# Kernel optimization log

Hardware: AMD Instinct MI355X
Metric: run time of the kernel (lower is better)

## Reference

```python
import jax, jax.numpy as jnp
import numpy as np

B, L, D, H = 4, 1024, 1024, 16
HD = D // H
TERM = 20  # N-term / C-term window size


def setup_inputs() -> dict:
    key = jax.random.key(0)
    ks = jax.random.split(key, 9)
    x = jax.random.normal(ks[0], (B, L, D), jnp.float32)
    lens = jax.random.randint(ks[1], (B,), 64, L + 1)
    mask = jnp.arange(L)[None, :] < lens[:, None]  # contiguous valid prefix, bool [B,L]
    s = 0.02  # ~ xavier_uniform with gain 1/H**0.25
    Wq = jax.random.normal(ks[2], (D, D), jnp.float32) * s
    Wk = jax.random.normal(ks[3], (D, D), jnp.float32) * s
    Wv = jax.random.normal(ks[4], (D, D), jnp.float32) * s
    bq = jnp.zeros((D,), jnp.float32)
    bk = jnp.zeros((D,), jnp.float32)
    bv = jnp.zeros((D,), jnp.float32)
    gamma = jnp.ones((D,), jnp.float32)
    beta = jnp.zeros((D,), jnp.float32)
    return {"x": x, "mask": mask, "Wq": Wq, "bq": bq, "Wk": Wk, "bk": bk,
            "Wv": Wv, "bv": bv, "gamma": gamma, "beta": beta}


def reference(x, mask, Wq, bq, Wk, bk, Wv, bv, gamma, beta):
    # LayerNorm (eps = 1e-5, torch default)
    mu = x.mean(-1, keepdims=True)
    var = ((x - mu) ** 2).mean(-1, keepdims=True)
    xn = (x - mu) / jnp.sqrt(var + 1e-5) * gamma + beta

    Q = (xn @ Wq + bq).reshape(B, L, H, HD)
    K = (xn @ Wk + bk).reshape(B, L, H, HD)
    V = (xn @ Wv + bv).reshape(B, L, H, HD)

    # note: original divides by head_dim**0.25 (quarter power) - keep faithful
    scores = jnp.einsum('bqhd,bkhd->bhqk', Q, K) / HD ** 0.25

    # mask fill on key positions
    scores = jnp.where(mask[:, None, None, :], scores, -10000.0)

    # per-sample length-dependent bias on key positions
    lens = mask.sum(-1)                      # [B] int
    pos = jnp.arange(L)                      # [L]
    inlen = pos[None, :] < lens[:, None]     # [B,L]
    bias_ge = (1.0 * (pos[None, :] < TERM)
               + 0.8 * ((pos[None, :] >= lens[:, None] - TERM) & inlen))
    bias_lt = (1.0 + 0.8) * inlen
    bias = jnp.where((lens >= TERM)[:, None], bias_ge, bias_lt)  # [B,L]
    scores = scores + bias[:, None, None, :]

    attn = jax.nn.softmax(scores, axis=-1)   # [B,H,L,L]
    entropy_loss = -(attn * jnp.log(attn + 1e-10)).sum(-1).mean()

    context = jnp.einsum('bhqk,bkhd->bqhd', attn, V).reshape(B, L, D)

    # ragged N-term / C-term mean pooling (vectorized segment means)
    term = jnp.minimum(TERM, lens)           # [B]
    termf = term.astype(x.dtype)[:, None]
    wn = (pos[None, :] < term[:, None]).astype(x.dtype)                      # first term tokens
    wc = ((pos[None, :] >= (lens - term)[:, None]) & inlen).astype(x.dtype)  # last term valid tokens
    n_term = (context * wn[:, :, None]).sum(1) / termf
    c_term = (context * wc[:, :, None]).sum(1) / termf
    global_pool = context.mean(1)            # mean over full L, as in original

    pooled = jnp.concatenate([n_term, c_term, global_pool], axis=1)  # [B,3D]
    return pooled, attn.mean(1), entropy_loss
```

## Files before the change

kernel.cpp:

```cpp
#include <hip/hip_runtime.h>
#include <hip/hip_bf16.h>
#include <hip/hip_fp16.h>


typedef unsigned short u16;
typedef __attribute__((ext_vector_type(4))) float f32x4;
typedef __attribute__((ext_vector_type(8))) __bf16 bf16x8;
typedef __attribute__((ext_vector_type(4))) unsigned int u32x4;
typedef __attribute__((ext_vector_type(4))) unsigned short u16x4;
typedef __attribute__((ext_vector_type(8))) unsigned short u16x8;

typedef const __attribute__((address_space(1))) unsigned int* gas1;
typedef __attribute__((address_space(3))) unsigned int* las3;

#define DEV __device__ __forceinline__

DEV float bf2f(u16 u){ union{unsigned i; float f;} c; c.i = ((unsigned)u)<<16; return c.f; }
DEV u16 f2bf(float f){ union{float f; unsigned i;} c; c.f=f; unsigned i=c.i;
  unsigned r = i + 0x7FFFu + ((i>>16)&1u); return (u16)(r>>16); }

__global__ void k_detect(const void* mask, const void* gamma, const void* beta,
                         const void* bq, const void* bk, const void* bv,
                         int* lens, float* ent, int* flag,
                         u16* gam_c, u16* bet_c, u16* bq_c, u16* bk_c, u16* bv_c,
                         float* pacc){
  int t = threadIdx.x; int w = t>>6; int lane = t&63;
  int isf32 = (((const u16*)gamma)[0] == 0) ? 1 : 0;
  if (t==0){ *flag = isf32; *ent = 0.f; }
  for (int i=t; i<12288; i+=256) pacc[i] = 0.f;
  for (int i=t; i<1024; i+=256){
    if (isf32){
      gam_c[i]=f2bf(((const float*)gamma)[i]); bet_c[i]=f2bf(((const float*)beta)[i]);
      bq_c[i] =f2bf(((const float*)bq)[i]);    bk_c[i] =f2bf(((const float*)bk)[i]);
      bv_c[i] =f2bf(((const float*)bv)[i]);
    } else {
      gam_c[i]=((const u16*)gamma)[i]; bet_c[i]=((const u16*)beta)[i];
      bq_c[i] =((const u16*)bq)[i];    bk_c[i] =((const u16*)bk)[i];
      bv_c[i] =((const u16*)bv)[i];
    }
  }
  const unsigned char* mb = (const unsigned char*)mask;
  const int* mi = (const int*)mask;
  const u16* ms = (const u16*)mask;
  int cnt = 0;
  if (mb[1] != 0) {
    if (mb[0]==1 && mb[1]==1) { for (int i=lane;i<1024;i+=64) cnt += (mb[w*1024+i]!=0); }
    else                      { for (int i=lane;i<1024;i+=64) cnt += (ms[w*1024+i]!=0); }
  } else {
    if (mi[1]==0)             { for (int i=lane;i<1024;i+=64) cnt += (mi[(w*1024+i)*2]!=0); }
    else                      { for (int i=lane;i<1024;i+=64) cnt += (mi[w*1024+i]!=0); }
  }
  #pragma unroll
  for (int o=32;o;o>>=1) cnt += __shfl_down(cnt,o);
  if (lane==0) lens[w] = cnt;
}

DEV void tr64_body(const void* src, u16* dst, int R, int C, int bt, int isf32, int t,
                   u16 (*tile)[68]){
  int tc_n = C>>6;
  int tr = (bt / tc_n)<<6, tc = (bt % tc_n)<<6;
  if (isf32){
    const float* s = (const float*)src;
    #pragma unroll
    for (int it=0; it<2; ++it){
      int f = it*2048 + t*8; int r=f>>6, c=f&63;
      const float* p = s + (long)(tr+r)*C + tc + c;
      f32x4 a = *(const f32x4*)p, b = *(const f32x4*)(p+4);
      u16x4 ua, ub;
      #pragma unroll
      for (int j=0;j<4;j++){ ua[j]=f2bf(a[j]); ub[j]=f2bf(b[j]); }
      *(u16x4*)&tile[r][c]   = ua;
      *(u16x4*)&tile[r][c+4] = ub;
    }
  } else {
    const u16* s = (const u16*)src;
    #pragma unroll
    for (int it=0; it<2; ++it){
      int f = it*2048 + t*8; int r=f>>6, c=f&63;
      *(u16x4*)&tile[r][c]   = *(const u16x4*)(s + (long)(tr+r)*C + tc + c);
      *(u16x4*)&tile[r][c+4] = *(const u16x4*)(s + (long)(tr+r)*C + tc + c + 4);
    }
  }
  __syncthreads();
  #pragma unroll
  for (int it=0; it<2; ++it){
    int f = it*2048 + t*8; int r=f>>6, c=f&63;
    u16x4 a, b2;
    #pragma unroll
    for (int j=0;j<4;j++){ a[j]=tile[c+j][r]; b2[j]=tile[c+4+j][r]; }
    *(u16x4*)(dst + (long)(tc+r)*R + tr + c)     = a;
    *(u16x4*)(dst + (long)(tc+r)*R + tr + c + 4) = b2;
  }
}

__global__ __launch_bounds__(256) void k_prep(const void* x, const u16* gamma, const u16* beta,
    u16* xn, const void* Wq, const void* Wk, const void* Wv, u16* Wt, const int* flagp){
  __shared__ u16 tile[64][68];
  int isf32 = *flagp;
  int id = blockIdx.x, t = threadIdx.x;
  if (id < 4096){
    int row = id;
    float f0,f1,f2,f3;
    if (isf32){
      f32x4 v = ((const f32x4*)x)[(size_t)row*256 + t];
      f0=v[0]; f1=v[1]; f2=v[2]; f3=v[3];
    } else {
      u16x4 v = ((const u16x4*)x)[(size_t)row*256 + t];
      f0=bf2f(v[0]); f1=bf2f(v[1]); f2=bf2f(v[2]); f3=bf2f(v[3]);
    }
    float s = f0+f1+f2+f3;
    float sq = f0*f0+f1*f1+f2*f2+f3*f3;
    #pragma unroll
    for (int o=32;o;o>>=1){ s += __shfl_down(s,o); sq += __shfl_down(sq,o); }
    float* rs = (float*)&tile[0][0];
    float* rq = rs + 4;
    if ((t&63)==0){ rs[t>>6]=s; rq[t>>6]=sq; }
    __syncthreads();
    s = rs[0]+rs[1]+rs[2]+rs[3]; sq = rq[0]+rq[1]+rq[2]+rq[3];
    float mu = s*(1.0f/1024.0f);
    float var = sq*(1.0f/1024.0f) - mu*mu;
    float rstd = rsqrtf(var + 1e-5f);
    u16x4 gv = ((const u16x4*)gamma)[t];
    u16x4 bv = ((const u16x4*)beta)[t];
    u16x4 o;
    o[0]=f2bf((f0-mu)*rstd*bf2f(gv[0])+bf2f(bv[0]));
    o[1]=f2bf((f1-mu)*rstd*bf2f(gv[1])+bf2f(bv[1]));
    o[2]=f2bf((f2-mu)*rstd*bf2f(gv[2])+bf2f(bv[2]));
    o[3]=f2bf((f3-mu)*rstd*bf2f(gv[3])+bf2f(bv[3]));
    ((u16x4*)(xn + (size_t)row*1024))[t] = o;
  } else {
    int bt = id - 4096;
    int sub = bt >> 8, tl = bt & 255;
    const void* src = (sub==0) ? Wq : (sub==1) ? Wk : Wv;
    tr64_body(src, Wt + ((size_t)sub<<20), 1024, 1024, tl, isf32, t, tile);
  }
}

__global__ __launch_bounds__(256) void k_trV(const u16* Vb, u16* Vt){
  __shared__ u16 tile[64][68];
  tr64_body(Vb + ((size_t)blockIdx.y<<16), Vt + ((size_t)blockIdx.y<<16),
            1024, 64, blockIdx.x, 0, threadIdx.x, tile);
}

__global__ __launch_bounds__(256) void k_gemm(const u16* A, const u16* Bt,
    const u16* biasq, const u16* biask, const u16* biasv,
    u16* Qb, u16* Kb, u16* Vb, const int* lens){
  int m0 = (blockIdx.x & 31)<<7;
  int n0 = (int)(blockIdx.x >> 5)<<7;
  if (n0 >= 1024 && (m0 & 1023) >= lens[m0>>10]) return;
  __shared__ u16 lA[2][4096];
  __shared__ u16 lB[2][4096];
  int t = threadIdx.x;
  int w = t>>6, l = t&63, g = l>>4, lc = l&15;
  int wm = w>>1, wn = w&1;
  int fb0 = t*16, fb1 = 4096 + t*16;
  int r0 = fb0>>6, c0 = fb0&63, r1 = fb1>>6, c1 = fb1&63;
  const char* Ab = (const char*)A; const char* Bb = (const char*)Bt;
  long aoff0 = (long)(m0+r0)*2048 + c0;
  long aoff1 = (long)(m0+r1)*2048 + c1;
  long boff0 = (long)(n0+r0)*2048 + c0;
  long boff1 = (long)(n0+r1)*2048 + c1;
  int lw = w<<10;

  #define STAGEK(buf, ko) do{ \
    __builtin_amdgcn_global_load_lds((gas1)(const void*)(Ab + aoff0 + (ko)), \
        (las3)(void*)((char*)&lA[buf][0] + lw), 16, 0, 0); \
    __builtin_amdgcn_global_load_lds((gas1)(const void*)(Ab + aoff1 + (ko)), \
        (las3)(void*)((char*)&lA[buf][0] + 4096 + lw), 16, 0, 0); \
    __builtin_amdgcn_global_load_lds((gas1)(const void*)(Bb + boff0 + (ko)), \
        (las3)(void*)((char*)&lB[buf][0] + lw), 16, 0, 0); \
    __builtin_amdgcn_global_load_lds((gas1)(const void*)(Bb + boff1 + (ko)), \
        (las3)(void*)((char*)&lB[buf][0] + 4096 + lw), 16, 0, 0); \
  }while(0)

  f32x4 vzero = {0.f,0.f,0.f,0.f};
  f32x4 acc[4][4];
  #pragma unroll
  for (int i=0;i<4;i++)
    #pragma unroll
    for (int j=0;j<4;j++) acc[i][j] = vzero;

  STAGEK(0, 0);
  __syncthreads();
  for (int kt=0; kt<32; ++kt){
    int cur = kt & 1;
    if (kt < 31) STAGEK(cur^1, (long)(kt+1)*64);
    bf16x8 af[4], bfr[4];
    #pragma unroll
    for (int i=0;i<4;i++) af[i]  = *(const bf16x8*)(const void*)&lA[cur][((wm<<6)+(i<<4)+lc)*32 + (g<<3)];
    #pragma unroll
    for (int j=0;j<4;j++) bfr[j] = *(const bf16x8*)(const void*)&lB[cur][((wn<<6)+(j<<4)+lc)*32 + (g<<3)];
    #pragma unroll
    for (int i=0;i<4;i++)
      #pragma unroll
      for (int j=0;j<4;j++)
        acc[i][j] = __builtin_amdgcn_mfma_f32_16x16x32_bf16(af[i], bfr[j], acc[i][j], 0,0,0);
    __syncthreads();
  }
  #undef STAGEK
  #pragma unroll
  for (int j=0;j<4;j++){
    int n = n0 + (wn<<6) + (j<<4) + lc;
    int kind = n>>10; int nn = n & 1023;
    const u16* bp = (kind==0)?biasq:(kind==1)?biask:biasv;
    float bvl = bf2f(bp[nn]);
    u16* dst = (kind==0)?Qb:(kind==1)?Kb:Vb;
    int h = nn>>6, hd = n&63;
    #pragma unroll
    for (int i=0;i<4;i++){
      #pragma unroll
      for (int r=0;r<4;r++){
        int m = m0 + (wm<<6) + (i<<4) + (g<<2) + r;
        int bb = m>>10, pos = m&1023;
        dst[(((bb<<4)+h)<<16) + (pos<<6) + hd] = f2bf(acc[i][j][r] + bvl);
      }
    }
  }
}

__global__ __launch_bounds__(512) void k_attn(const u16* Qg, const u16* Kg, const u16* Vt,
    const int* lens, u16* ctx, u16* Pp, float* ent_acc){
  __shared__ u16 Plds[16][1032];
  __shared__ float redz[16][8];
  __shared__ float rede[16][8];
  __shared__ __half redc[2][16][66];
  int bqi = blockIdx.x;
  int qt = bqi & 63, hg = (bqi>>6)&3, b = bqi>>8;
  int q0 = qt<<4;
  int t = threadIdx.x, w = t>>6, l = t&63, g = l>>4, lc = l&15;
  int kh = w>>2, dg = w&3;
  int len = lens[b];
  {
    u16x8 z8 = {0,0,0,0,0,0,0,0};
    u16* pz = &Plds[0][0];
    for (int i=t; i<2064; i+=512) *(u16x8*)(pz + i*8) = z8;
  }
  __half2 mh[8][2];
  #pragma unroll
  for (int i=0;i<8;i++){ mh[i][0] = __float2half2_rn(0.f); mh[i][1] = __float2half2_rn(0.f); }
  float ent_local = 0.f;
  const float SCALE = 0.35355339059327373f;
  for (int hh=0; hh<4; ++hh){
    int h = (hg<<2) + hh;
    int base = ((b<<4)+h)<<16;
    bf16x8 qf0 = *(const bf16x8*)(const void*)(Qg + base + ((q0+lc)<<6) + (g<<3));
    bf16x8 qf1 = *(const bf16x8*)(const void*)(Qg + base + ((q0+lc)<<6) + (g<<3) + 32);
    f32x4 s[8];
    float zp[4]={0,0,0,0}, ep[4]={0,0,0,0};
    #pragma unroll
    for (int tt=0; tt<8; ++tt){
      int kb = (tt<<7)+(w<<4);
      if (kb < len){
        const u16* kp = Kg + base + ((kb+lc)<<6) + (g<<3);
        bf16x8 kf0 = *(const bf16x8*)(const void*)kp;
        bf16x8 kf1 = *(const bf16x8*)(const void*)(kp + 32);
        f32x4 a = {0.f,0.f,0.f,0.f};
        a = __builtin_amdgcn_mfma_f32_16x16x32_bf16(qf0, kf0, a, 0,0,0);
        a = __builtin_amdgcn_mfma_f32_16x16x32_bf16(qf1, kf1, a, 0,0,0);
        int key = kb + lc;
        bool valid = key < len;
        float bias;
        if (len >= 20) bias = (key<20 ? 1.0f : 0.0f) + ((valid && key >= len-20) ? 0.8f : 0.0f);
        else bias = 1.8f;
        #pragma unroll
        for (int r=0;r<4;r++){
          float sv = valid ? a[r]*SCALE + bias : -10000.0f;
          float e = __expf(fminf(sv, 60.0f));
          zp[r]+=e; ep[r]+=e*sv;
          a[r] = e;
          Plds[(g<<2)+r][key] = f2bf(e);
        }
        s[tt] = a;
      }
    }
    #pragma unroll
    for (int r=0;r<4;r++){
      zp[r]+=__shfl_xor(zp[r],1); ep[r]+=__shfl_xor(ep[r],1);
      zp[r]+=__shfl_xor(zp[r],2); ep[r]+=__shfl_xor(ep[r],2);
      zp[r]+=__shfl_xor(zp[r],4); ep[r]+=__shfl_xor(ep[r],4);
      zp[r]+=__shfl_xor(zp[r],8); ep[r]+=__shfl_xor(ep[r],8);
    }
    if (lc==0){
      #pragma unroll
      for (int r=0;r<4;r++){ redz[(g<<2)+r][w]=zp[r]; rede[(g<<2)+r][w]=ep[r]; }
    }
    __syncthreads();
    float invz[4];
    #pragma unroll
    for (int r=0;r<4;r++){
      int rr=(g<<2)+r;
      float Z = redz[rr][0]+redz[rr][1]+redz[rr][2]+redz[rr][3]
              + redz[rr][4]+redz[rr][5]+redz[rr][6]+redz[rr][7];
      float E = rede[rr][0]+rede[rr][1]+rede[rr][2]+rede[rr][3]
              + rede[rr][4]+rede[rr][5]+rede[rr][6]+rede[rr][7];
      invz[r] = 1.0f/Z;
      if (w==0 && lc==0) ent_local += __logf(Z) - E*invz[r];
    }
    #pragma unroll
    for (int tt=0;tt<8;++tt){
      if (((tt<<7)+(w<<4)) < len){
        float p0 = s[tt][0]*invz[0], p1 = s[tt][1]*invz[1];
        float p2 = s[tt][2]*invz[2], p3 = s[tt][3]*invz[3];
        mh[tt][0] = __hadd2(mh[tt][0], __halves2half2(__float2half_rn(p0), __float2half_rn(p1)));
        mh[tt][1] = __hadd2(mh[tt][1], __halves2half2(__float2half_rn(p2), __float2half_rn(p3)));
      }
    }
    f32x4 cacc = {0.f,0.f,0.f,0.f};
    const u16* vrow = Vt + base + (((dg<<4)+lc)<<10);
    #pragma unroll
    for (int ks=0; ks<16; ++ks){
      int kk = (ks<<1)+kh;
      if ((kk<<5) < len){
        bf16x8 pa = *(const bf16x8*)(const void*)(&Plds[0][0] + lc*1032 + (kk<<5) + (g<<3));
        bf16x8 vb = *(const bf16x8*)(const void*)(vrow + (kk<<5) + (g<<3));
        cacc = __builtin_amdgcn_mfma_f32_16x16x32_bf16(pa, vb, cacc, 0,0,0);
      }
    }
    #pragma unroll
    for (int r=0;r<4;r++) redc[kh][(g<<2)+r][(dg<<4)+lc] = __float2half(cacc[r]*invz[r]);
    __syncthreads();
    #pragma unroll
    for (int ii=0; ii<2; ++ii){
      int i = t + (ii<<9);
      int q = i>>6, d = i&63;
      float v = __half2float(redc[0][q][d]) + __half2float(redc[1][q][d]);
      ctx[(((size_t)(b<<10)+q0+q)<<10) + (h<<6) + d] = f2bf(v);
    }
  }
  u16* oa = Pp + ((size_t)hg<<22) + ((size_t)b<<20);
  #pragma unroll
  for (int tt=0; tt<8; ++tt){
    int col = (tt<<7)+(w<<4)+lc;
    int qb_ = (q0+(g<<2))<<10;
    oa[qb_ + col]            = __half_as_ushort(__low2half(mh[tt][0]));
    oa[qb_ + 1024 + col]     = __half_as_ushort(__high2half(mh[tt][0]));
    oa[qb_ + 2048 + col]     = __half_as_ushort(__low2half(mh[tt][1]));
    oa[qb_ + 3072 + col]     = __half_as_ushort(__high2half(mh[tt][1]));
  }
  if (w==0){
    float es = ent_local;
    #pragma unroll
    for (int o=32;o;o>>=1) es += __shfl_down(es,o);
    if (l==0) atomicAdd(ent_acc, es);
  }
}

__global__ __launch_bounds__(256) void k_pmix(const u16* Pp, void* out_v, const int* flagp,
                                              const u16* ctx, const int* lens, float* pacc){
  int id = blockIdx.x;
  if (id < 2048){
    int isf32 = *flagp;
    size_t idx = ((size_t)id*256 + threadIdx.x)*8;
    int b = (int)(idx>>20); size_t f = idx & 0xFFFFFu;
    const u16* p0 = Pp + ((size_t)b<<20) + f;
    float s[8] = {0,0,0,0,0,0,0,0};
    #pragma unroll
    for (int gI=0; gI<4; ++gI){
      u16x8 v = *(const u16x8*)(p0 + ((size_t)gI<<22));
      #pragma unroll
      for (int j=0;j<8;j++) s[j] += __half2float(__ushort_as_half(v[j]));
    }
    if (isf32){
      float* o = (float*)out_v + 12288 + idx;
      #pragma unroll
      for (int j=0;j<8;j++) o[j] = s[j]*0.0625f;
    } else {
      u16x8 o;
      #pragma unroll
      for (int j=0;j<8;j++) o[j] = f2bf(s[j]*0.0625f);
      *(u16x8*)((u16*)out_v + 12288 + idx) = o;
    }
  } else {
    int pid = id - 2048;
    int b = pid>>5, pc = pid&31;
    int t = threadIdx.x; int d0 = t*4;
    int len = lens[b];
    int term = len < 20 ? len : 20;
    int lo = len - term;
    float sn[4]={0,0,0,0}, sc[4]={0,0,0,0}, sg[4]={0,0,0,0};
    const u16* base = ctx + ((size_t)b<<20) + ((size_t)pc<<15) + d0;
    for (int p=0;p<32;++p){
      int gp = (pc<<5)+p;
      u16x4 v = *(const u16x4*)(base + ((size_t)p<<10));
      bool in_n = gp < term;
      bool in_c = (gp >= lo) && (gp < len);
      #pragma unroll
      for (int j=0;j<4;j++){
        float fv = bf2f(v[j]);
        sg[j] += fv;
        if (in_n) sn[j] += fv;
        if (in_c) sc[j] += fv;
      }
    }
    #pragma unroll
    for (int j=0;j<4;j++){
      atomicAdd(&pacc[(b<<10)+d0+j], sn[j]);
      atomicAdd(&pacc[4096+(b<<10)+d0+j], sc[j]);
      atomicAdd(&pacc[8192+(b<<10)+d0+j], sg[j]);
    }
  }
}

__global__ __launch_bounds__(256) void k_pool2(const float* pacc, const int* lens, const float* ent,
                                               void* out_v, const int* flagp){
  int isf32 = *flagp;
  int idx = blockIdx.x*256 + threadIdx.x;
  if (idx < 12288){
    int b = idx/3072; int r = idx - b*3072; int seg = r>>10; int d = r&1023;
    int len = lens[b]; int term = len < 20 ? len : 20;
    float scale = (seg==2) ? (1.0f/1024.0f) : (1.0f/(float)term);
    float v = pacc[seg*4096 + (b<<10) + d]*scale;
    if (isf32) ((float*)out_v)[idx] = v; else ((u16*)out_v)[idx] = f2bf(v);
  }
  if (idx==0){
    float e = (*ent)*(1.0f/65536.0f);
    if (isf32) ((float*)out_v)[4206592] = e; else ((u16*)out_v)[4206592] = f2bf(e);
  }
}

extern "C" void kernel_launch(void* const* d_in, const int* in_sizes, int n_in,
                              void* d_out, int out_size, void* d_ws, size_t ws_size,
                              hipStream_t stream){
  (void)in_sizes; (void)n_in; (void)out_size; (void)ws_size;
  const void* x     = d_in[0];
  const void* mask  = d_in[1];
  const void* Wq    = d_in[2];
  const void* bq    = d_in[3];
  const void* Wk    = d_in[4];
  const void* bk    = d_in[5];
  const void* Wv    = d_in[6];
  const void* bv    = d_in[7];
  const void* gamma = d_in[8];
  const void* beta  = d_in[9];

  char* ws = (char*)d_ws;
  int*   lens = (int*)ws;
  float* ent  = (float*)(ws + 64);
  int*   flag = (int*)(ws + 68);
  u16* gam_c = (u16*)(ws + 256);
  u16* bet_c = gam_c + 1024;
  u16* bq_c  = bet_c + 1024;
  u16* bk_c  = bq_c + 1024;
  u16* bv_c  = bk_c + 1024;
  u16* xn  = (u16*)(ws + 0x100000);
  u16* Qb  = (u16*)(ws + 0x900000);
  u16* Kb  = (u16*)(ws + 0x1100000);
  u16* ctx = (u16*)(ws + 0x1900000);
  u16* Pp  = (u16*)(ws + 0x2100000);
  u16* Wt  = (u16*)(ws + 0x2100000);
  u16* Vb  = (u16*)(ws + 0x2700000);
  u16* Vt  = xn;
  float* pacc = (float*)(ws + 0x4100000);

  k_detect<<<1,256,0,stream>>>(mask, gamma, beta, bq, bk, bv,
                               lens, ent, flag, gam_c, bet_c, bq_c, bk_c, bv_c, pacc);
  k_prep<<<4864,256,0,stream>>>(x, gam_c, bet_c, xn, Wq, Wk, Wv, Wt, flag);
  k_gemm<<<768,256,0,stream>>>(xn, Wt, bq_c, bk_c, bv_c, Qb, Kb, Vb, lens);
  k_trV<<<dim3(16,64),256,0,stream>>>(Vb, Vt);
  k_attn<<<1024,512,0,stream>>>(Qb, Kb, Vt, lens, ctx, Pp, ent);
  k_pmix<<<2176,256,0,stream>>>(Pp, d_out, flag, ctx, lens, pacc);
  k_pool2<<<49,256,0,stream>>>(pacc, lens, ent, d_out, flag);
}
```

Before: 165.3 us.

## Fold detect kernel into prep and use persistent atomic tile scheduler in GEMM

Removes the single-block k_detect launch by moving mask-length counting, bias conversion and accumulator zeroing into an extra block of k_prep, with gamma/beta read directly in their native dtype. The QKV GEMM becomes a persistent kernel of 512 blocks that pulls tile indices from a global atomic counter, skipping masked V/K tiles without leaving idle blocks. This saves one launch and evens out GEMM work, at the cost of an atomic and extra barriers per tile.

```diff
diff --git a/kernel.cpp b/kernel.cpp
--- a/kernel.cpp
+++ b/kernel.cpp
@@ -19,42 +19,6 @@
 DEV u16 f2bf(float f){ union{float f; unsigned i;} c; c.f=f; unsigned i=c.i;
   unsigned r = i + 0x7FFFu + ((i>>16)&1u); return (u16)(r>>16); }
 
-__global__ void k_detect(const void* mask, const void* gamma, const void* beta,
-                         const void* bq, const void* bk, const void* bv,
-                         int* lens, float* ent, int* flag,
-                         u16* gam_c, u16* bet_c, u16* bq_c, u16* bk_c, u16* bv_c,
-                         float* pacc){
-  int t = threadIdx.x; int w = t>>6; int lane = t&63;
-  int isf32 = (((const u16*)gamma)[0] == 0) ? 1 : 0;
-  if (t==0){ *flag = isf32; *ent = 0.f; }
-  for (int i=t; i<12288; i+=256) pacc[i] = 0.f;
-  for (int i=t; i<1024; i+=256){
-    if (isf32){
-      gam_c[i]=f2bf(((const float*)gamma)[i]); bet_c[i]=f2bf(((const float*)beta)[i]);
-      bq_c[i] =f2bf(((const float*)bq)[i]);    bk_c[i] =f2bf(((const float*)bk)[i]);
-      bv_c[i] =f2bf(((const float*)bv)[i]);
-    } else {
-      gam_c[i]=((const u16*)gamma)[i]; bet_c[i]=((const u16*)beta)[i];
-      bq_c[i] =((const u16*)bq)[i];    bk_c[i] =((const u16*)bk)[i];
-      bv_c[i] =((const u16*)bv)[i];
-    }
-  }
-  const unsigned char* mb = (const unsigned char*)mask;
-  const int* mi = (const int*)mask;
-  const u16* ms = (const u16*)mask;
-  int cnt = 0;
-  if (mb[1] != 0) {
-    if (mb[0]==1 && mb[1]==1) { for (int i=lane;i<1024;i+=64) cnt += (mb[w*1024+i]!=0); }
-    else                      { for (int i=lane;i<1024;i+=64) cnt += (ms[w*1024+i]!=0); }
-  } else {
-    if (mi[1]==0)             { for (int i=lane;i<1024;i+=64) cnt += (mi[(w*1024+i)*2]!=0); }
-    else                      { for (int i=lane;i<1024;i+=64) cnt += (mi[w*1024+i]!=0); }
-  }
-  #pragma unroll
-  for (int o=32;o;o>>=1) cnt += __shfl_down(cnt,o);
-  if (lane==0) lens[w] = cnt;
-}
-
 DEV void tr64_body(const void* src, u16* dst, int R, int C, int bt, int isf32, int t,
                    u16 (*tile)[68]){
   int tc_n = C>>6;
@@ -93,10 +57,13 @@
   }
 }
 
-__global__ __launch_bounds__(256) void k_prep(const void* x, const u16* gamma, const u16* beta,
-    u16* xn, const void* Wq, const void* Wk, const void* Wv, u16* Wt, const int* flagp){
+__global__ __launch_bounds__(256) void k_prep(const void* x, const void* gamma, const void* beta,
+    u16* xn, const void* Wq, const void* Wk, const void* Wv, u16* Wt,
+    const void* mask, const void* bq, const void* bk, const void* bv,
+    int* lens, float* ent, int* flag, int* cnt,
+    u16* bq_c, u16* bk_c, u16* bv_c, float* pacc){
   __shared__ u16 tile[64][68];
-  int isf32 = *flagp;
+  int isf32 = (((const u16*)gamma)[0] == 0) ? 1 : 0;
   int id = blockIdx.x, t = threadIdx.x;
   if (id < 4096){
     int row = id;
@@ -120,19 +87,53 @@
     float mu = s*(1.0f/1024.0f);
     float var = sq*(1.0f/1024.0f) - mu*mu;
     float rstd = rsqrtf(var + 1e-5f);
-    u16x4 gv = ((const u16x4*)gamma)[t];
-    u16x4 bv = ((const u16x4*)beta)[t];
+    float gv[4], bv4[4];
+    if (isf32){
+      f32x4 gg = ((const f32x4*)gamma)[t]; f32x4 bb = ((const f32x4*)beta)[t];
+      #pragma unroll
+      for (int j=0;j<4;j++){ gv[j]=gg[j]; bv4[j]=bb[j]; }
+    } else {
+      u16x4 gg = ((const u16x4*)gamma)[t]; u16x4 bb = ((const u16x4*)beta)[t];
+      #pragma unroll
+      for (int j=0;j<4;j++){ gv[j]=bf2f(gg[j]); bv4[j]=bf2f(bb[j]); }
+    }
     u16x4 o;
-    o[0]=f2bf((f0-mu)*rstd*bf2f(gv[0])+bf2f(bv[0]));
-    o[1]=f2bf((f1-mu)*rstd*bf2f(gv[1])+bf2f(bv[1]));
-    o[2]=f2bf((f2-mu)*rstd*bf2f(gv[2])+bf2f(bv[2]));
-    o[3]=f2bf((f3-mu)*rstd*bf2f(gv[3])+bf2f(bv[3]));
+    o[0]=f2bf((f0-mu)*rstd*gv[0]+bv4[0]);
+    o[1]=f2bf((f1-mu)*rstd*gv[1]+bv4[1]);
+    o[2]=f2bf((f2-mu)*rstd*gv[2]+bv4[2]);
+    o[3]=f2bf((f3-mu)*rstd*gv[3]+bv4[3]);
     ((u16x4*)(xn + (size_t)row*1024))[t] = o;
-  } else {
+  } else if (id < 4864){
     int bt = id - 4096;
     int sub = bt >> 8, tl = bt & 255;
     const void* src = (sub==0) ? Wq : (sub==1) ? Wk : Wv;
     tr64_body(src, Wt + ((size_t)sub<<20), 1024, 1024, tl, isf32, t, tile);
+  } else {
+    int w = t>>6, lane = t&63;
+    if (t==0){ *flag = isf32; *ent = 0.f; *cnt = 0; }
+    for (int i=t; i<12288; i+=256) pacc[i] = 0.f;
+    for (int i=t; i<1024; i+=256){
+      if (isf32){
+        bq_c[i]=f2bf(((const float*)bq)[i]); bk_c[i]=f2bf(((const float*)bk)[i]);
+        bv_c[i]=f2bf(((const float*)bv)[i]);
+      } else {
+        bq_c[i]=((const u16*)bq)[i]; bk_c[i]=((const u16*)bk)[i]; bv_c[i]=((const u16*)bv)[i];
+      }
+    }
+    const unsigned char* mb = (const unsigned char*)mask;
+    const int* mi = (const int*)mask;
+    const u16* ms = (const u16*)mask;
+    int cntv = 0;
+    if (mb[1] != 0) {
+      if (mb[0]==1 && mb[1]==1) { for (int i=lane;i<1024;i+=64) cntv += (mb[w*1024+i]!=0); }
+      else                      { for (int i=lane;i<1024;i+=64) cntv += (ms[w*1024+i]!=0); }
+    } else {
+      if (mi[1]==0)             { for (int i=lane;i<1024;i+=64) cntv += (mi[(w*1024+i)*2]!=0); }
+      else                      { for (int i=lane;i<1024;i+=64) cntv += (mi[w*1024+i]!=0); }
+    }
+    #pragma unroll
+    for (int o=32;o;o>>=1) cntv += __shfl_down(cntv,o);
+    if (lane==0) lens[w] = cntv;
   }
 }
 
@@ -144,22 +145,16 @@
 
 __global__ __launch_bounds__(256) void k_gemm(const u16* A, const u16* Bt,
     const u16* biasq, const u16* biask, const u16* biasv,
-    u16* Qb, u16* Kb, u16* Vb, const int* lens){
-  int m0 = (blockIdx.x & 31)<<7;
-  int n0 = (int)(blockIdx.x >> 5)<<7;
-  if (n0 >= 1024 && (m0 & 1023) >= lens[m0>>10]) return;
+    u16* Qb, u16* Kb, u16* Vb, const int* lens, int* cnt){
   __shared__ u16 lA[2][4096];
   __shared__ u16 lB[2][4096];
+  __shared__ int sidx;
   int t = threadIdx.x;
   int w = t>>6, l = t&63, g = l>>4, lc = l&15;
   int wm = w>>1, wn = w&1;
   int fb0 = t*16, fb1 = 4096 + t*16;
   int r0 = fb0>>6, c0 = fb0&63, r1 = fb1>>6, c1 = fb1&63;
   const char* Ab = (const char*)A; const char* Bb = (const char*)Bt;
-  long aoff0 = (long)(m0+r0)*2048 + c0;
-  long aoff1 = (long)(m0+r1)*2048 + c1;
-  long boff0 = (long)(n0+r0)*2048 + c0;
-  long boff1 = (long)(n0+r1)*2048 + c1;
   int lw = w<<10;
 
   #define STAGEK(buf, ko) do{ \
@@ -173,49 +168,62 @@
         (las3)(void*)((char*)&lB[buf][0] + 4096 + lw), 16, 0, 0); \
   }while(0)
 
-  f32x4 vzero = {0.f,0.f,0.f,0.f};
-  f32x4 acc[4][4];
-  #pragma unroll
-  for (int i=0;i<4;i++)
-    #pragma unroll
-    for (int j=0;j<4;j++) acc[i][j] = vzero;
-
-  STAGEK(0, 0);
-  __syncthreads();
-  for (int kt=0; kt<32; ++kt){
-    int cur = kt & 1;
-    if (kt < 31) STAGEK(cur^1, (long)(kt+1)*64);
-    bf16x8 af[4], bfr[4];
-    #pragma unroll
-    for (int i=0;i<4;i++) af[i]  = *(const bf16x8*)(const void*)&lA[cur][((wm<<6)+(i<<4)+lc)*32 + (g<<3)];
-    #pragma unroll
-    for (int j=0;j<4;j++) bfr[j] = *(const bf16x8*)(const void*)&lB[cur][((wn<<6)+(j<<4)+lc)*32 + (g<<3)];
+  for(;;){
+    __syncthreads();
+    if (t==0) sidx = atomicAdd(cnt, 1);
+    __syncthreads();
+    int bid = sidx;
+    if (bid >= 768) return;
+    int m0 = (bid & 31)<<7;
+    int n0 = (bid >> 5)<<7;
+    if (n0 >= 1024 && (m0 & 1023) >= lens[m0>>10]) continue;
+    long aoff0 = (long)(m0+r0)*2048 + c0;
+    long aoff1 = (long)(m0+r1)*2048 + c1;
+    long boff0 = (long)(n0+r0)*2048 + c0;
+    long boff1 = (long)(n0+r1)*2048 + c1;
+    f32x4 vzero = {0.f,0.f,0.f,0.f};
+    f32x4 acc[4][4];
     #pragma unroll
     for (int i=0;i<4;i++)
       #pragma unroll
-      for (int j=0;j<4;j++)
-        acc[i][j] = __builtin_amdgcn_mfma_f32_16x16x32_bf16(af[i], bfr[j], acc[i][j], 0,0,0);
-    __syncthreads();
+      for (int j=0;j<4;j++) acc[i][j] = vzero;
+    STAGEK(0, 0);
+    __syncthreads();
+    for (int kt=0; kt<32; ++kt){
+      int cur = kt & 1;
+      if (kt < 31) STAGEK(cur^1, (long)(kt+1)*64);
+      bf16x8 af[4], bfr[4];
+      #pragma unroll
+      for (int i=0;i<4;i++) af[i]  = *(const bf16x8*)(const void*)&lA[cur][((wm<<6)+(i<<4)+lc)*32 + (g<<3)];
+      #pragma unroll
+      for (int j=0;j<4;j++) bfr[j] = *(const bf16x8*)(const void*)&lB[cur][((wn<<6)+(j<<4)+lc)*32 + (g<<3)];
+      #pragma unroll
+      for (int i=0;i<4;i++)
+        #pragma unroll
+        for (int j=0;j<4;j++)
+          acc[i][j] = __builtin_amdgcn_mfma_f32_16x16x32_bf16(af[i], bfr[j], acc[i][j], 0,0,0);
+      __syncthreads();
+    }
+    #pragma unroll
+    for (int j=0;j<4;j++){
+      int n = n0 + (wn<<6) + (j<<4) + lc;
+      int kind = n>>10; int nn = n & 1023;
+      const u16* bp = (kind==0)?biasq:(kind==1)?biask:biasv;
+      float bvl = bf2f(bp[nn]);
+      u16* dst = (kind==0)?Qb:(kind==1)?Kb:Vb;
+      int h = nn>>6, hd = n&63;
+      #pragma unroll
+      for (int i=0;i<4;i++){
+        #pragma unroll
+        for (int r=0;r<4;r++){
+          int m = m0 + (wm<<6) + (i<<4) + (g<<2) + r;
+          int bb = m>>10, pos = m&1023;
+          dst[(((bb<<4)+h)<<16) + (pos<<6) + hd] = f2bf(acc[i][j][r] + bvl);
+        }
+      }
+    }
   }
   #undef STAGEK
-  #pragma unroll
-  for (int j=0;j<4;j++){
-    int n = n0 + (wn<<6) + (j<<4) + lc;
-    int kind = n>>10; int nn = n & 1023;
-    const u16* bp = (kind==0)?biasq:(kind==1)?biask:biasv;
-    float bvl = bf2f(bp[nn]);
-    u16* dst = (kind==0)?Qb:(kind==1)?Kb:Vb;
-    int h = nn>>6, hd = n&63;
-    #pragma unroll
-    for (int i=0;i<4;i++){
-      #pragma unroll
-      for (int r=0;r<4;r++){
-        int m = m0 + (wm<<6) + (i<<4) + (g<<2) + r;
-        int bb = m>>10, pos = m&1023;
-        dst[(((bb<<4)+h)<<16) + (pos<<6) + hd] = f2bf(acc[i][j][r] + bvl);
-      }
-    }
-  }
 }
 
 __global__ __launch_bounds__(512) void k_attn(const u16* Qg, const u16* Kg, const u16* Vt,
@@ -437,9 +445,8 @@
   int*   lens = (int*)ws;
   float* ent  = (float*)(ws + 64);
   int*   flag = (int*)(ws + 68);
-  u16* gam_c = (u16*)(ws + 256);
-  u16* bet_c = gam_c + 1024;
-  u16* bq_c  = bet_c + 1024;
+  int*   cnt  = (int*)(ws + 72);
+  u16* bq_c  = (u16*)(ws + 256);
   u16* bk_c  = bq_c + 1024;
   u16* bv_c  = bk_c + 1024;
   u16* xn  = (u16*)(ws + 0x100000);
@@ -452,10 +459,10 @@
   u16* Vt  = xn;
   float* pacc = (float*)(ws + 0x4100000);
 
-  k_detect<<<1,256,0,stream>>>(mask, gamma, beta, bq, bk, bv,
-                               lens, ent, flag, gam_c, bet_c, bq_c, bk_c, bv_c, pacc);
-  k_prep<<<4864,256,0,stream>>>(x, gam_c, bet_c, xn, Wq, Wk, Wv, Wt, flag);
-  k_gemm<<<768,256,0,stream>>>(xn, Wt, bq_c, bk_c, bv_c, Qb, Kb, Vb, lens);
+  k_prep<<<4865,256,0,stream>>>(x, gamma, beta, xn, Wq, Wk, Wv, Wt,
+                                mask, bq, bk, bv, lens, ent, flag, cnt,
+                                bq_c, bk_c, bv_c, pacc);
+  k_gemm<<<512,256,0,stream>>>(xn, Wt, bq_c, bk_c, bv_c, Qb, Kb, Vb, lens, cnt);
   k_trV<<<dim3(16,64),256,0,stream>>>(Vb, Vt);
   k_attn<<<1024,512,0,stream>>>(Qb, Kb, Vt, lens, ctx, Pp, ent);
   k_pmix<<<2176,256,0,stream>>>(Pp, d_out, flag, ctx, lens, pacc);
```

Measured after the change: 187.2 us. 13.2% more time.
